# Kernel optimization log

Measured on AMD Instinct MI355X. Metric: run time of the kernel, lower is better.

Reference implementation:

```python
import jax, jax.numpy as jnp
import numpy as np
import math

NUM_LAYERS = 4
NHEAD = 8
D_MODEL = 256
EPS_ATTN = 1e-6
EPS_LN = 1e-5


def _pos_encoding(d_model, h, w, dtype):
    # LoFTR 2D sinusoidal pos-enc, sliced to (h, w)
    d4 = d_model // 4
    y_pos = jnp.arange(1, h + 1, dtype=dtype)[None, :, None]  # [1,h,1]
    x_pos = jnp.arange(1, w + 1, dtype=dtype)[None, None, :]  # [1,1,w]
    div = jnp.exp(jnp.arange(0, d_model // 2, 2, dtype=dtype) * (-math.log(10000.0) / (d_model // 2)))
    div = div[:, None, None]  # [d4,1,1]
    pe = jnp.zeros((d_model, h, w), dtype=dtype)
    pe = pe.at[0::4].set(jnp.sin(x_pos * div))
    pe = pe.at[1::4].set(jnp.cos(x_pos * div))
    pe = pe.at[2::4].set(jnp.sin(y_pos * div))
    pe = pe.at[3::4].set(jnp.cos(y_pos * div))
    return pe


def _layernorm(x, g, b):
    mu = jnp.mean(x, axis=-1, keepdims=True)
    var = jnp.mean(jnp.square(x - mu), axis=-1, keepdims=True)
    return (x - mu) * jax.lax.rsqrt(var + EPS_LN) * g + b


def _encoder_layer(x, Wq, Wk, Wv, Wm, W1, W2, g1, b1, g2, b2):
    # x: [n, L, d]; weights stored [in, out]
    n, L, d = x.shape
    dh = d // NHEAD
    q = (x @ Wq).reshape(n, L, NHEAD, dh)
    k = (x @ Wk).reshape(n, L, NHEAD, dh)
    v = (x @ Wv).reshape(n, L, NHEAD, dh)
    # linear attention: feature map elu(x)+1
    Q = jax.nn.elu(q) + 1.0
    K = jax.nn.elu(k) + 1.0
    v_len = jnp.asarray(L, x.dtype)
    V = v / v_len
    KV = jnp.einsum('nshd,nshv->nhdv', K, V)            # [n,H,dh,dh]
    Z = 1.0 / (jnp.einsum('nlhd,nhd->nlh', Q, K.sum(axis=1)) + EPS_ATTN)
    msg = jnp.einsum('nlhd,nhdv,nlh->nlhv', Q, KV, Z) * v_len  # [n,L,H,dh]
    msg = msg.reshape(n, L, d) @ Wm
    msg = _layernorm(msg, g1, b1)
    msg = jnp.concatenate([x, msg], axis=-1)             # [n,L,2d]
    msg = jax.nn.relu(msg @ W1) @ W2
    msg = _layernorm(msg, g2, b2)
    return x + msg


def setup_inputs() -> dict:
    key = jax.random.key(0)
    ks = jax.random.split(key, 8)
    b, c, h, w = 8, D_MODEL, 64, 64
    d = D_MODEL
    sc_d = 1.0 / math.sqrt(d)
    sc_2d = 1.0 / math.sqrt(2 * d)
    feats = jax.random.normal(ks[0], (b, c, h, w), dtype=jnp.float32)
    Wq = jax.random.normal(ks[1], (NUM_LAYERS, d, d), dtype=jnp.float32) * sc_d
    Wk = jax.random.normal(ks[2], (NUM_LAYERS, d, d), dtype=jnp.float32) * sc_d
    Wv = jax.random.normal(ks[3], (NUM_LAYERS, d, d), dtype=jnp.float32) * sc_d
    Wmerge = jax.random.normal(ks[4], (NUM_LAYERS, d, d), dtype=jnp.float32) * sc_d
    Wmlp1 = jax.random.normal(ks[5], (NUM_LAYERS, 2 * d, 2 * d), dtype=jnp.float32) * sc_2d
    Wmlp2 = jax.random.normal(ks[6], (NUM_LAYERS, 2 * d, d), dtype=jnp.float32) * sc_2d
    ln1_g = jnp.ones((NUM_LAYERS, d), dtype=jnp.float32)
    ln1_b = jnp.zeros((NUM_LAYERS, d), dtype=jnp.float32)
    ln2_g = jnp.ones((NUM_LAYERS, d), dtype=jnp.float32)
    ln2_b = jnp.zeros((NUM_LAYERS, d), dtype=jnp.float32)
    return {'feats': feats, 'Wq': Wq, 'Wk': Wk, 'Wv': Wv, 'Wmerge': Wmerge,
            'Wmlp1': Wmlp1, 'Wmlp2': Wmlp2, 'ln1_g': ln1_g, 'ln1_b': ln1_b,
            'ln2_g': ln2_g, 'ln2_b': ln2_b}


def reference(feats, Wq, Wk, Wv, Wmerge, Wmlp1, Wmlp2, ln1_g, ln1_b, ln2_g, ln2_b):
    b, c, h, w = feats.shape
    x = feats + _pos_encoding(c, h, w, feats.dtype)[None]   # add_posEnc=True
    x = x.reshape(b, c, h * w).transpose(0, 2, 1)            # n (h w) c
    for i in range(NUM_LAYERS):
        x = _encoder_layer(x, Wq[i], Wk[i], Wv[i], Wmerge[i], Wmlp1[i], Wmlp2[i],
                           ln1_g[i], ln1_b[i], ln2_g[i], ln2_b[i])
    return x.transpose(0, 2, 1).reshape(b, c, h, w)
```

## Files before the change

kernel.cpp:

```cpp
#include <hip/hip_runtime.h>
#include <hip/hip_bf16.h>

#define LTOT 4096
#define DM 256
#define BATCH 8
#define MROWS (BATCH * LTOT)
#define NX ((size_t)MROWS * DM)

typedef __bf16 bf16x8 __attribute__((ext_vector_type(8)));
typedef float f32x4 __attribute__((ext_vector_type(4)));

#define AS1 __attribute__((address_space(1)))
#define AS3 __attribute__((address_space(3)))

__device__ __forceinline__ float elu1(float x) {
    return x > 0.f ? x + 1.f : expf(x);
}
__device__ __forceinline__ ushort f2bf(float f) {
    unsigned u = __float_as_uint(f);
    u += 0x7FFFu + ((u >> 16) & 1u);
    return (ushort)(u >> 16);
}
__device__ __forceinline__ float b2f(ushort u) {
    return __uint_as_float(((unsigned)u) << 16);
}

__global__ __launch_bounds__(256) void prep_kernel(const float* __restrict__ feats,
                                                   ushort* __restrict__ XC) {
    __shared__ float tile[32][33];
    int b = blockIdx.z;
    int l0 = blockIdx.x * 32;
    int c0 = blockIdx.y * 32;
    int tx = threadIdx.x, ty = threadIdx.y;
#pragma unroll
    for (int j = 0; j < 4; ++j) {
        int c = c0 + ty + j * 8;
        tile[ty + j * 8][tx] = feats[((size_t)(b * DM + c)) * LTOT + l0 + tx];
    }
    __syncthreads();
#pragma unroll
    for (int j = 0; j < 4; ++j) {
        int l = l0 + ty + j * 8;
        int c = c0 + tx;
        int i2 = (c >> 2) * 2;
        float dv = expf((float)i2 * -0.07195578415156063f);
        int rem = c & 3;
        int y = l >> 6, xc = l & 63;
        float pos = (rem < 2) ? (float)(xc + 1) : (float)(y + 1);
        float arg = pos * dv;
        float pe = (rem & 1) ? cosf(arg) : sinf(arg);
        float val = tile[tx][ty + j * 8] + pe;
        size_t row = (size_t)(b * LTOT + l);
        XC[row * 512 + c] = f2bf(val);
    }
}

__global__ __launch_bounds__(256) void unprep_kernel(const float* __restrict__ X,
                                                     float* __restrict__ out) {
    __shared__ float tile[32][33];
    int b = blockIdx.z;
    int l0 = blockIdx.x * 32;
    int c0 = blockIdx.y * 32;
    int tx = threadIdx.x, ty = threadIdx.y;
#pragma unroll
    for (int j = 0; j < 4; ++j) {
        int l = l0 + ty + j * 8;
        tile[ty + j * 8][tx] = X[((size_t)(b * LTOT + l)) * DM + c0 + tx];
    }
    __syncthreads();
#pragma unroll
    for (int j = 0; j < 4; ++j) {
        int c = c0 + ty + j * 8;
        out[((size_t)(b * DM + c)) * LTOT + l0 + tx] = tile[tx][ty + j * 8];
    }
}

__global__ __launch_bounds__(256) void wtrans_all(const float* __restrict__ Wq,
                                                  const float* __restrict__ Wk,
                                                  const float* __restrict__ Wv,
                                                  const float* __restrict__ Wm,
                                                  const float* __restrict__ W1,
                                                  const float* __restrict__ W2,
                                                  ushort* __restrict__ WTqkv,
                                                  ushort* __restrict__ WTm,
                                                  ushort* __restrict__ WT1,
                                                  ushort* __restrict__ WT2) {
    __shared__ float t[32][33];
    int idx = blockIdx.x;
    const float* W;
    ushort* WT;
    int K, N, KT, z, r;
    size_t in_ls, out_ls;
    if (idx < 1024) {
        int which = idx >> 8, local = idx & 255;
        K = 256; N = 256; KT = 8; in_ls = 65536;
        if (which == 0)      { W = Wq; WT = WTqkv;          out_ls = 196608; }
        else if (which == 1) { W = Wk; WT = WTqkv + 65536;  out_ls = 196608; }
        else if (which == 2) { W = Wv; WT = WTqkv + 131072; out_ls = 196608; }
        else                 { W = Wm; WT = WTm;            out_ls = 65536; }
        z = local >> 6; r = local & 63;
    } else if (idx < 2048) {
        int local = idx - 1024;
        K = 512; N = 512; KT = 16; in_ls = 262144; out_ls = 262144;
        W = W1; WT = WT1;
        z = local >> 8; r = local & 255;
    } else {
        int local = idx - 2048;
        K = 512; N = 256; KT = 16; in_ls = 131072; out_ls = 131072;
        W = W2; WT = WT2;
        z = local >> 7; r = local & 127;
    }
    int k0 = (r % KT) * 32, n0 = (r / KT) * 32;
    const float* Wz = W + (size_t)z * in_ls;
    ushort* WTz = WT + (size_t)z * out_ls;
    int tx = threadIdx.x & 31, ty = threadIdx.x >> 5;
#pragma unroll
    for (int j = 0; j < 4; ++j)
        t[ty + j * 8][tx] = Wz[(size_t)(k0 + ty + j * 8) * N + n0 + tx];
    __syncthreads();
#pragma unroll
    for (int j = 0; j < 4; ++j)
        WTz[(size_t)(n0 + ty + j * 8) * K + k0 + tx] = f2bf(t[tx][ty + j * 8]);
}

template <int ACT, int K>
__global__ __launch_bounds__(512, 2) void gemm_bf16(const ushort* __restrict__ A, int lda,
                                                    const ushort* __restrict__ Bt,
                                                    ushort* __restrict__ Cb,
                                                    int N) {
    constexpr int S = K / 32;
    __shared__ ushort As[3][4096];
    __shared__ ushort Bs[3][8192];
    int tid = threadIdx.x;
    int m0 = blockIdx.x * 128, n0 = blockIdx.y * 256;
    int wave = tid >> 6, lane = tid & 63;
    int wm = (wave >> 2) * 64, wn = (wave & 3) * 64;
    int fm = lane & 15, kg = lane >> 4;
    int rr = tid >> 2;
    int cc = (((tid & 3) - (tid >> 3)) & 3) * 8;
    int sa = ((kg + (fm >> 1)) & 3) * 8;

    const ushort* Ag = A + (size_t)(m0 + rr) * lda + cc;
    const ushort* Bg = Bt + (size_t)(n0 + rr) * K + cc;
    const ushort* Bg2 = Bt + (size_t)(n0 + rr + 128) * K + cc;

    f32x4 acc[4][4] = {};

#define STAGE_G(buf, k0)                                                          \
    do {                                                                          \
        __builtin_amdgcn_global_load_lds((const AS1 void*)(Ag + (k0)),            \
                                         (AS3 void*)(&As[buf][wave * 512]),       \
                                         16, 0, 0);                               \
        __builtin_amdgcn_global_load_lds((const AS1 void*)(Bg + (k0)),            \
                                         (AS3 void*)(&Bs[buf][wave * 512]),       \
                                         16, 0, 0);                               \
        __builtin_amdgcn_global_load_lds((const AS1 void*)(Bg2 + (k0)),           \
                                         (AS3 void*)(&Bs[buf][4096 + wave * 512]),\
                                         16, 0, 0);                               \
    } while (0)

    STAGE_G(0, 0);
    STAGE_G(1, 32);
#pragma unroll
    for (int t = 0; t < S; ++t) {
        if (t + 1 < S) asm volatile("s_waitcnt vmcnt(3)" ::: "memory");
        else           asm volatile("s_waitcnt vmcnt(0)" ::: "memory");
        __builtin_amdgcn_s_barrier();
        const int rb = t % 3;
        bf16x8 afr[4], bfr[4];
#pragma unroll
        for (int i = 0; i < 4; ++i)
            afr[i] = *(const bf16x8*)(&As[rb][(wm + i * 16 + fm) * 32 + sa]);
#pragma unroll
        for (int j = 0; j < 4; ++j)
            bfr[j] = *(const bf16x8*)(&Bs[rb][(wn + j * 16 + fm) * 32 + sa]);
        if (t + 2 < S) STAGE_G((t + 2) % 3, (t + 2) * 32);
#pragma unroll
        for (int i = 0; i < 4; ++i)
#pragma unroll
            for (int j = 0; j < 4; ++j)
                acc[i][j] = __builtin_amdgcn_mfma_f32_16x16x32_bf16(afr[i], bfr[j], acc[i][j], 0, 0, 0);
        asm volatile("" ::: "memory");
        __builtin_amdgcn_s_barrier();
    }
#undef STAGE_G

#pragma unroll
    for (int i = 0; i < 4; ++i) {
        int grow0 = m0 + wm + i * 16 + kg * 4;
#pragma unroll
        for (int r = 0; r < 4; ++r) {
            size_t rowoff = (size_t)(grow0 + r) * N;
#pragma unroll
            for (int j = 0; j < 4; ++j) {
                float v = acc[i][j][r];
                int col = n0 + wn + j * 16 + fm;
                if (ACT == 2) v = fmaxf(v, 0.f);
                if (ACT == 3) v = (col < 512) ? elu1(v) : v;
                Cb[rowoff + col] = f2bf(v);
            }
        }
    }
}

template <int RES, int K>
__global__ __launch_bounds__(512, 2) void gemm_ln(const ushort* __restrict__ A, int lda,
                                                  const ushort* __restrict__ Bt,
                                                  const float* __restrict__ g,
                                                  const float* __restrict__ bta,
                                                  float* __restrict__ Xout,
                                                  ushort* __restrict__ XC) {
    constexpr int S = K / 32;
    __shared__ ushort As[3][4096];
    __shared__ ushort Bs[3][8192];
    __shared__ float red[128 * 8];
    __shared__ float musig[128 * 2];
    int tid = threadIdx.x;
    int m0 = blockIdx.x * 128;
    int wave = tid >> 6, lane = tid & 63;
    int wm = (wave >> 2) * 64, wn = (wave & 3) * 64;
    int fm = lane & 15, kg = lane >> 4;
    int rr = tid >> 2;
    int cc = (((tid & 3) - (tid >> 3)) & 3) * 8;
    int sa = ((kg + (fm >> 1)) & 3) * 8;

    const ushort* Ag = A + (size_t)(m0 + rr) * lda + cc;
    const ushort* Bg = Bt + (size_t)rr * K + cc;
    const ushort* Bg2 = Bt + (size_t)(rr + 128) * K + cc;

    f32x4 acc[4][4] = {};

#define STAGE_L(buf, k0)                                                          \
    do {                                                                          \
        __builtin_amdgcn_global_load_lds((const AS1 void*)(Ag + (k0)),            \
                                         (AS3 void*)(&As[buf][wave * 512]),       \
                                         16, 0, 0);                               \
        __builtin_amdgcn_global_load_lds((const AS1 void*)(Bg + (k0)),            \
                                         (AS3 void*)(&Bs[buf][wave * 512]),       \
                                         16, 0, 0);                               \
        __builtin_amdgcn_global_load_lds((const AS1 void*)(Bg2 + (k0)),           \
                                         (AS3 void*)(&Bs[buf][4096 + wave * 512]),\
                                         16, 0, 0);                               \
    } while (0)

    STAGE_L(0, 0);
    STAGE_L(1, 32);
#pragma unroll
    for (int t = 0; t < S; ++t) {
        if (t + 1 < S) asm volatile("s_waitcnt vmcnt(3)" ::: "memory");
        else           asm volatile("s_waitcnt vmcnt(0)" ::: "memory");
        __builtin_amdgcn_s_barrier();
        const int rb = t % 3;
        bf16x8 afr[4], bfr[4];
#pragma unroll
        for (int i = 0; i < 4; ++i)
            afr[i] = *(const bf16x8*)(&As[rb][(i * 16 + fm + wm) * 32 + sa]);
#pragma unroll
        for (int j = 0; j < 4; ++j)
            bfr[j] = *(const bf16x8*)(&Bs[rb][(wn + j * 16 + fm) * 32 + sa]);
        if (t + 2 < S) STAGE_L((t + 2) % 3, (t + 2) * 32);
#pragma unroll
        for (int i = 0; i < 4; ++i)
#pragma unroll
            for (int j = 0; j < 4; ++j)
                acc[i][j] = __builtin_amdgcn_mfma_f32_16x16x32_bf16(afr[i], bfr[j], acc[i][j], 0, 0, 0);
        asm volatile("" ::: "memory");
        __builtin_amdgcn_s_barrier();
    }
#undef STAGE_L

#pragma unroll
    for (int i = 0; i < 4; ++i) {
#pragma unroll
        for (int r = 0; r < 4; ++r) {
            float s = acc[i][0][r] + acc[i][1][r] + acc[i][2][r] + acc[i][3][r];
            float q = acc[i][0][r] * acc[i][0][r] + acc[i][1][r] * acc[i][1][r] +
                      acc[i][2][r] * acc[i][2][r] + acc[i][3][r] * acc[i][3][r];
#pragma unroll
            for (int o = 1; o < 16; o <<= 1) {
                s += __shfl_xor(s, o, 64);
                q += __shfl_xor(q, o, 64);
            }
            if ((lane & 15) == 0) {
                int row = wm + i * 16 + kg * 4 + r;
                red[row * 8 + (wave & 3)] = s;
                red[row * 8 + 4 + (wave & 3)] = q;
            }
        }
    }
    __syncthreads();
    if (tid < 128) {
        float s = red[tid * 8 + 0] + red[tid * 8 + 1] + red[tid * 8 + 2] + red[tid * 8 + 3];
        float q = red[tid * 8 + 4] + red[tid * 8 + 5] + red[tid * 8 + 6] + red[tid * 8 + 7];
        float mu = s * (1.f / 256.f);
        float var = q * (1.f / 256.f) - mu * mu;
        musig[tid * 2] = mu;
        musig[tid * 2 + 1] = rsqrtf(var + 1e-5f);
    }
    __syncthreads();

    float gv[4], bv[4];
#pragma unroll
    for (int j = 0; j < 4; ++j) {
        int col = wn + j * 16 + fm;
        gv[j] = g[col];
        bv[j] = bta[col];
    }
#pragma unroll
    for (int i = 0; i < 4; ++i) {
#pragma unroll
        for (int r = 0; r < 4; ++r) {
            int rl = wm + i * 16 + kg * 4 + r;
            float mu = musig[rl * 2], rstd = musig[rl * 2 + 1];
            size_t grow = (size_t)(m0 + rl);
#pragma unroll
            for (int j = 0; j < 4; ++j) {
                int col = wn + j * 16 + fm;
                float v = (acc[i][j][r] - mu) * rstd * gv[j] + bv[j];
                if (RES) {
                    float x = b2f(XC[grow * 512 + col]) + v;
                    XC[grow * 512 + col] = f2bf(x);
                    if (Xout) Xout[grow * 256 + col] = x;
                } else {
                    XC[grow * 512 + 256 + col] = f2bf(v);
                }
            }
        }
    }
}

__global__ __launch_bounds__(256) void kv_kernel(const ushort* __restrict__ Kf,
                                                 const ushort* __restrict__ Vf,
                                                 int str,
                                                 float* __restrict__ KVp,
                                                 float* __restrict__ KSp) {
    __shared__ float redv[3][8][8][16];
    __shared__ float redk[3][8][4];
    int tid = threadIdx.x;
    int bh = blockIdx.x, sp = blockIdx.y;
    int b = bh >> 3, h = bh & 7;
    int sg = tid >> 6, d2 = (tid >> 3) & 7, v2 = tid & 7;
    size_t rbase = (size_t)(b * LTOT + sp * 512 + sg * 128) * str;
    const ushort* Kp = Kf + rbase + h * 32 + d2 * 4;
    const ushort* Vp = Vf + rbase + h * 32 + v2 * 4;
    float acc[4][4] = {};
    float ks[4] = {};
#pragma unroll 4
    for (int s = 0; s < 128; ++s) {
        ushort4 k4 = *(const ushort4*)(Kp + (size_t)s * str);
        ushort4 v4 = *(const ushort4*)(Vp + (size_t)s * str);
        float kk0 = b2f(k4.x), kk1 = b2f(k4.y), kk2 = b2f(k4.z), kk3 = b2f(k4.w);
        float vv0 = b2f(v4.x), vv1 = b2f(v4.y), vv2 = b2f(v4.z), vv3 = b2f(v4.w);
        acc[0][0] += kk0 * vv0; acc[0][1] += kk0 * vv1; acc[0][2] += kk0 * vv2; acc[0][3] += kk0 * vv3;
        acc[1][0] += kk1 * vv0; acc[1][1] += kk1 * vv1; acc[1][2] += kk1 * vv2; acc[1][3] += kk1 * vv3;
        acc[2][0] += kk2 * vv0; acc[2][1] += kk2 * vv1; acc[2][2] += kk2 * vv2; acc[2][3] += kk2 * vv3;
        acc[3][0] += kk3 * vv0; acc[3][1] += kk3 * vv1; acc[3][2] += kk3 * vv2; acc[3][3] += kk3 * vv3;
        ks[0] += kk0; ks[1] += kk1; ks[2] += kk2; ks[3] += kk3;
    }
    if (sg > 0) {
#pragma unroll
        for (int i = 0; i < 4; ++i)
#pragma unroll
            for (int j = 0; j < 4; ++j)
                redv[sg - 1][d2][v2][i * 4 + j] = acc[i][j];
        if (v2 == 0) {
#pragma unroll
            for (int i = 0; i < 4; ++i) redk[sg - 1][d2][i] = ks[i];
        }
    }
    __syncthreads();
    if (sg == 0) {
#pragma unroll
        for (int t = 0; t < 3; ++t)
#pragma unroll
            for (int i = 0; i < 4; ++i)
#pragma unroll
                for (int j = 0; j < 4; ++j)
                    acc[i][j] += redv[t][d2][v2][i * 4 + j];
        float* base = KVp + (size_t)(sp * 64 + bh) * 1024;
#pragma unroll
        for (int i = 0; i < 4; ++i) {
            float4 o = make_float4(acc[i][0], acc[i][1], acc[i][2], acc[i][3]);
            *(float4*)(base + (d2 * 4 + i) * 32 + v2 * 4) = o;
        }
        if (v2 == 0) {
#pragma unroll
            for (int t = 0; t < 3; ++t)
#pragma unroll
                for (int i = 0; i < 4; ++i) ks[i] += redk[t][d2][i];
#pragma unroll
            for (int i = 0; i < 4; ++i)
                KSp[(sp * 64 + bh) * 32 + d2 * 4 + i] = ks[i];
        }
    }
}

__global__ __launch_bounds__(256) void kvreduce_kernel(const float* __restrict__ KVp,
                                                       const float* __restrict__ KSp,
                                                       ushort* __restrict__ KVT,
                                                       float* __restrict__ KS) {
    int bh = blockIdx.x;
    int t = threadIdx.x;
    float4 s = make_float4(0.f, 0.f, 0.f, 0.f);
#pragma unroll
    for (int sp = 0; sp < 8; ++sp) {
        float4 v = *(const float4*)(KVp + ((size_t)(sp * 64 + bh)) * 1024 + t * 4);
        s.x += v.x; s.y += v.y; s.z += v.z; s.w += v.w;
    }
    int d = t >> 3, v0 = (t & 7) * 4;
    ushort* dst = KVT + (size_t)bh * 1024 + d;
    dst[(v0 + 0) * 32] = f2bf(s.x);
    dst[(v0 + 1) * 32] = f2bf(s.y);
    dst[(v0 + 2) * 32] = f2bf(s.z);
    dst[(v0 + 3) * 32] = f2bf(s.w);
    if (t < 32) {
        float ks = 0.f;
#pragma unroll
        for (int sp = 0; sp < 8; ++sp) ks += KSp[(sp * 64 + bh) * 32 + t];
        KS[bh * 32 + t] = ks;
    }
}

__global__ __launch_bounds__(256) void msg_mfma(const ushort* __restrict__ Qb, int qstr,
                                                const ushort* __restrict__ KVT,
                                                const float* __restrict__ KS,
                                                ushort* __restrict__ Msgb) {
    __shared__ ushort kvs[8 * 1280];
    int tid = threadIdx.x;
    int b = blockIdx.y;
    int lc = blockIdx.x;
    {
        const ushort* src = KVT + (size_t)b * 8192;
#pragma unroll
        for (int it = 0; it < 4; ++it) {
            int base = it * 2048 + tid * 8;
            int h = base >> 10, rem = base & 1023;
            int v = rem >> 5, d = rem & 31;
            bf16x8 val = *(const bf16x8*)(src + base);
            *(bf16x8*)(kvs + h * 1280 + v * 40 + d) = val;
        }
    }
    __syncthreads();
    int wave = tid >> 6, lane = tid & 63;
    int fm = lane & 15, kg = lane >> 4;
    int row0 = b * LTOT + lc * 64 + wave * 16;

    for (int h = 0; h < 8; ++h) {
        bf16x8 afr = *(const bf16x8*)(Qb + (size_t)(row0 + fm) * qstr + h * 32 + kg * 8);
        bf16x8 bfr0 = *(const bf16x8*)(kvs + h * 1280 + fm * 40 + kg * 8);
        bf16x8 bfr1 = *(const bf16x8*)(kvs + h * 1280 + (16 + fm) * 40 + kg * 8);
        f32x4 acc0 = {}, acc1 = {};
        acc0 = __builtin_amdgcn_mfma_f32_16x16x32_bf16(afr, bfr0, acc0, 0, 0, 0);
        acc1 = __builtin_amdgcn_mfma_f32_16x16x32_bf16(afr, bfr1, acc1, 0, 0, 0);
        const float* ksp = KS + (b * 8 + h) * 32 + kg * 8;
        float4 ka = *(const float4*)ksp;
        float4 kb = *(const float4*)(ksp + 4);
        float den = (float)afr[0] * ka.x + (float)afr[1] * ka.y +
                    (float)afr[2] * ka.z + (float)afr[3] * ka.w +
                    (float)afr[4] * kb.x + (float)afr[5] * kb.y +
                    (float)afr[6] * kb.z + (float)afr[7] * kb.w;
        den += __shfl_xor(den, 16, 64);
        den += __shfl_xor(den, 32, 64);
        float rz = 1.f / (den + 1e-6f);
#pragma unroll
        for (int r = 0; r < 4; ++r) {
            int rr = kg * 4 + r;
            float rzr = __shfl(rz, (kg << 4) | rr, 64);
            size_t ro = (size_t)(row0 + rr) * DM + h * 32;
            Msgb[ro + fm] = f2bf(acc0[r] * rzr);
            Msgb[ro + 16 + fm] = f2bf(acc1[r] * rzr);
        }
    }
}

extern "C" void kernel_launch(void* const* d_in, const int* in_sizes, int n_in,
                              void* d_out, int out_size, void* d_ws, size_t ws_size,
                              hipStream_t stream) {
    const float* feats = (const float*)d_in[0];
    const float* Wq = (const float*)d_in[1];
    const float* Wk = (const float*)d_in[2];
    const float* Wv = (const float*)d_in[3];
    const float* Wm = (const float*)d_in[4];
    const float* W1 = (const float*)d_in[5];
    const float* W2 = (const float*)d_in[6];
    const float* g1 = (const float*)d_in[7];
    const float* b1 = (const float*)d_in[8];
    const float* g2 = (const float*)d_in[9];
    const float* b2 = (const float*)d_in[10];

    float* ws = (float*)d_ws;
    float* X = ws;
    ushort* XC = (ushort*)(ws + NX);
    ushort* QKVb = (ushort*)(ws + 2 * NX);
    ushort* HBb = QKVb;

    float* dout = (float*)d_out;
    ushort* msgb = (ushort*)dout;
    ushort* WB = (ushort*)dout + NX;
    ushort* WTqkv = WB;
    ushort* WTm = WB + 4 * 196608;
    ushort* WT1 = WTm + 4 * 65536;
    ushort* WT2 = WT1 + 4 * 262144;
    float* KVp = dout + (NX + 2621440) / 2;
    float* KSp = KVp + 524288;
    ushort* KVT = (ushort*)(KSp + 16384);
    float* KS = (float*)(KVT + 65536);

    wtrans_all<<<2560, 256, 0, stream>>>(Wq, Wk, Wv, Wm, W1, W2, WTqkv, WTm, WT1, WT2);
    prep_kernel<<<dim3(128, 8, 8), dim3(32, 8), 0, stream>>>(feats, XC);

    for (int layer = 0; layer < 4; ++layer) {
        const ushort* wtqkv = WTqkv + (size_t)layer * 196608;
        const ushort* wtm = WTm + (size_t)layer * 65536;
        const ushort* wt1 = WT1 + (size_t)layer * 262144;
        const ushort* wt2 = WT2 + (size_t)layer * 131072;
        const float* lg1 = g1 + layer * DM;
        const float* lb1 = b1 + layer * DM;
        const float* lg2 = g2 + layer * DM;
        const float* lb2 = b2 + layer * DM;

        gemm_bf16<3, 256><<<dim3(256, 3), 512, 0, stream>>>(XC, 512, wtqkv, QKVb, 768);
        kv_kernel<<<dim3(64, 8), 256, 0, stream>>>(QKVb + 256, QKVb + 512, 768, KVp, KSp);
        kvreduce_kernel<<<64, 256, 0, stream>>>(KVp, KSp, KVT, KS);
        msg_mfma<<<dim3(64, 8), 256, 0, stream>>>(QKVb, 768, KVT, KS, msgb);
        gemm_ln<0, 256><<<256, 512, 0, stream>>>(msgb, 256, wtm, lg1, lb1, nullptr, XC);
        gemm_bf16<2, 512><<<dim3(256, 2), 512, 0, stream>>>(XC, 512, wt1, HBb, 512);
        gemm_ln<1, 512><<<256, 512, 0, stream>>>(HBb, 512, wt2, lg2, lb2,
                                                 (layer == 3) ? X : nullptr, XC);
    }

    unprep_kernel<<<dim3(128, 8, 8), dim3(32, 8), 0, stream>>>(X, dout);
}
```

Before: 647.9 us.

## Fuse KV partial reduction into msg kernel and drop trailing GEMM barrier

Removes the separate kvreduce kernel. Each msg_mfma block now sums the eight split partials of KV and K-sum for its batch and writes the bf16 transposed KV and the K-sum straight into shared memory. This saves one launch and a global round trip per layer. In exchange, every block redundantly re-reads the fp32 partials, which adds L2 traffic. Separately, both bf16 GEMM main loops drop the end-of-iteration barrier and rely on triple buffering plus the leading barrier to keep buffer reuse safe.

```diff
diff --git a/kernel.cpp b/kernel.cpp
--- a/kernel.cpp
+++ b/kernel.cpp
@@ -166,6 +166,7 @@
         if (t + 1 < S) asm volatile("s_waitcnt vmcnt(3)" ::: "memory");
         else           asm volatile("s_waitcnt vmcnt(0)" ::: "memory");
         __builtin_amdgcn_s_barrier();
+        asm volatile("" ::: "memory");
         const int rb = t % 3;
         bf16x8 afr[4], bfr[4];
 #pragma unroll
@@ -180,8 +181,6 @@
 #pragma unroll
             for (int j = 0; j < 4; ++j)
                 acc[i][j] = __builtin_amdgcn_mfma_f32_16x16x32_bf16(afr[i], bfr[j], acc[i][j], 0, 0, 0);
-        asm volatile("" ::: "memory");
-        __builtin_amdgcn_s_barrier();
     }
 #undef STAGE_G
 
@@ -250,6 +249,7 @@
         if (t + 1 < S) asm volatile("s_waitcnt vmcnt(3)" ::: "memory");
         else           asm volatile("s_waitcnt vmcnt(0)" ::: "memory");
         __builtin_amdgcn_s_barrier();
+        asm volatile("" ::: "memory");
         const int rb = t % 3;
         bf16x8 afr[4], bfr[4];
 #pragma unroll
@@ -264,8 +264,6 @@
 #pragma unroll
             for (int j = 0; j < 4; ++j)
                 acc[i][j] = __builtin_amdgcn_mfma_f32_16x16x32_bf16(afr[i], bfr[j], acc[i][j], 0, 0, 0);
-        asm volatile("" ::: "memory");
-        __builtin_amdgcn_s_barrier();
     }
 #undef STAGE_L
 
@@ -395,50 +393,38 @@
     }
 }
 
-__global__ __launch_bounds__(256) void kvreduce_kernel(const float* __restrict__ KVp,
-                                                       const float* __restrict__ KSp,
-                                                       ushort* __restrict__ KVT,
-                                                       float* __restrict__ KS) {
-    int bh = blockIdx.x;
-    int t = threadIdx.x;
-    float4 s = make_float4(0.f, 0.f, 0.f, 0.f);
-#pragma unroll
-    for (int sp = 0; sp < 8; ++sp) {
-        float4 v = *(const float4*)(KVp + ((size_t)(sp * 64 + bh)) * 1024 + t * 4);
-        s.x += v.x; s.y += v.y; s.z += v.z; s.w += v.w;
-    }
-    int d = t >> 3, v0 = (t & 7) * 4;
-    ushort* dst = KVT + (size_t)bh * 1024 + d;
-    dst[(v0 + 0) * 32] = f2bf(s.x);
-    dst[(v0 + 1) * 32] = f2bf(s.y);
-    dst[(v0 + 2) * 32] = f2bf(s.z);
-    dst[(v0 + 3) * 32] = f2bf(s.w);
-    if (t < 32) {
-        float ks = 0.f;
-#pragma unroll
-        for (int sp = 0; sp < 8; ++sp) ks += KSp[(sp * 64 + bh) * 32 + t];
-        KS[bh * 32 + t] = ks;
-    }
-}
-
 __global__ __launch_bounds__(256) void msg_mfma(const ushort* __restrict__ Qb, int qstr,
-                                                const ushort* __restrict__ KVT,
-                                                const float* __restrict__ KS,
+                                                const float* __restrict__ KVp,
+                                                const float* __restrict__ KSp,
                                                 ushort* __restrict__ Msgb) {
     __shared__ ushort kvs[8 * 1280];
+    __shared__ float ksl[8 * 32];
     int tid = threadIdx.x;
     int b = blockIdx.y;
     int lc = blockIdx.x;
     {
-        const ushort* src = KVT + (size_t)b * 8192;
-#pragma unroll
-        for (int it = 0; it < 4; ++it) {
-            int base = it * 2048 + tid * 8;
-            int h = base >> 10, rem = base & 1023;
-            int v = rem >> 5, d = rem & 31;
-            bf16x8 val = *(const bf16x8*)(src + base);
-            *(bf16x8*)(kvs + h * 1280 + v * 40 + d) = val;
-        }
+        int h = tid >> 5, t5 = tid & 31;
+        const float* src = KVp + (size_t)(b * 8 + h) * 1024;
+#pragma unroll
+        for (int it = 0; it < 8; ++it) {
+            int q4 = t5 * 8 + it;
+            float4 s = make_float4(0.f, 0.f, 0.f, 0.f);
+#pragma unroll
+            for (int sp = 0; sp < 8; ++sp) {
+                float4 v = *(const float4*)(src + (size_t)sp * 65536 + q4 * 4);
+                s.x += v.x; s.y += v.y; s.z += v.z; s.w += v.w;
+            }
+            int d = q4 >> 3, v0 = (q4 & 7) * 4;
+            ushort* dst = kvs + h * 1280 + d;
+            dst[(v0 + 0) * 40] = f2bf(s.x);
+            dst[(v0 + 1) * 40] = f2bf(s.y);
+            dst[(v0 + 2) * 40] = f2bf(s.z);
+            dst[(v0 + 3) * 40] = f2bf(s.w);
+        }
+        float ks = 0.f;
+#pragma unroll
+        for (int sp = 0; sp < 8; ++sp) ks += KSp[(sp * 64 + b * 8 + h) * 32 + t5];
+        ksl[tid] = ks;
     }
     __syncthreads();
     int wave = tid >> 6, lane = tid & 63;
@@ -452,7 +438,7 @@
         f32x4 acc0 = {}, acc1 = {};
         acc0 = __builtin_amdgcn_mfma_f32_16x16x32_bf16(afr, bfr0, acc0, 0, 0, 0);
         acc1 = __builtin_amdgcn_mfma_f32_16x16x32_bf16(afr, bfr1, acc1, 0, 0, 0);
-        const float* ksp = KS + (b * 8 + h) * 32 + kg * 8;
+        const float* ksp = ksl + h * 32 + kg * 8;
         float4 ka = *(const float4*)ksp;
         float4 kb = *(const float4*)(ksp + 4);
         float den = (float)afr[0] * ka.x + (float)afr[1] * ka.y +
@@ -503,8 +489,6 @@
     ushort* WT2 = WT1 + 4 * 262144;
     float* KVp = dout + (NX + 2621440) / 2;
     float* KSp = KVp + 524288;
-    ushort* KVT = (ushort*)(KSp + 16384);
-    float* KS = (float*)(KVT + 65536);
 
     wtrans_all<<<2560, 256, 0, stream>>>(Wq, Wk, Wv, Wm, W1, W2, WTqkv, WTm, WT1, WT2);
     prep_kernel<<<dim3(128, 8, 8), dim3(32, 8), 0, stream>>>(feats, XC);
@@ -521,8 +505,7 @@
 
         gemm_bf16<3, 256><<<dim3(256, 3), 512, 0, stream>>>(XC, 512, wtqkv, QKVb, 768);
         kv_kernel<<<dim3(64, 8), 256, 0, stream>>>(QKVb + 256, QKVb + 512, 768, KVp, KSp);
-        kvreduce_kernel<<<64, 256, 0, stream>>>(KVp, KSp, KVT, KS);
-        msg_mfma<<<dim3(64, 8), 256, 0, stream>>>(QKVb, 768, KVT, KS, msgb);
+        msg_mfma<<<dim3(64, 8), 256, 0, stream>>>(QKVb, 768, KVp, KSp, msgb);
         gemm_ln<0, 256><<<256, 512, 0, stream>>>(msgb, 256, wtm, lg1, lb1, nullptr, XC);
         gemm_bf16<2, 512><<<dim3(256, 2), 512, 0, stream>>>(XC, 512, wt1, HBb, 512);
         gemm_ln<1, 512><<<256, 512, 0, stream>>>(HBb, 512, wt2, lg2, lb2,
```

Measured after the change: 725.7 us. 12.0% more time.
